# Kernel optimization log

Hardware: AMD Instinct MI355X
Metric: run time of the kernel (lower is better)

The kernel has to match this reference:

```python
import jax, jax.numpy as jnp
import numpy as np

NEG_SLOPE = 0.01


def conv2d_border(x, w, b, stride):
    # replicate ('border') padding of 1, then VALID conv; matches torch padding_mode='border'
    x = jnp.pad(x, ((0, 0), (0, 0), (1, 1), (1, 1)), mode='edge')
    y = jax.lax.conv_general_dilated(x, w, (stride, stride), 'VALID',
                                     dimension_numbers=('NCHW', 'OIHW', 'NCHW'))
    return y + b[None, :, None, None]


def leaky(x):
    return jnp.where(x >= 0, x, NEG_SLOPE * x)


def view_encoder(x, w1, b1, w2, b2, w3, b3):
    x = leaky(conv2d_border(x, w1, b1, 1))
    x = leaky(conv2d_border(x, w2, b2, 2))
    x = leaky(conv2d_border(x, w3, b3, 2))
    return x  # (V, F, H/4, W/4)


def bilinear_gather(nts, uv, vid):
    # nts: (V, F, Hp, Wp); uv: (N, 2) in [0,1]; vid: (N,) int -> (N, F)
    V, Fd, Hp, Wp = nts.shape
    tex = jnp.transpose(nts, (0, 2, 3, 1))  # (V, Hp, Wp, F)
    x = uv[:, 0] * (Wp - 1)
    y = uv[:, 1] * (Hp - 1)
    x0 = jnp.clip(jnp.floor(x).astype(jnp.int32), 0, Wp - 2)
    y0 = jnp.clip(jnp.floor(y).astype(jnp.int32), 0, Hp - 2)
    wx = (x - x0)[:, None]
    wy = (y - y0)[:, None]
    f00 = tex[vid, y0, x0]
    f01 = tex[vid, y0, x0 + 1]
    f10 = tex[vid, y0 + 1, x0]
    f11 = tex[vid, y0 + 1, x0 + 1]
    return (f00 * (1 - wx) * (1 - wy) + f01 * wx * (1 - wy)
            + f10 * (1 - wx) * wy + f11 * wx * wy)


def mha(q, k, v, wq, bq, wk, bk, wv, bv, wo, bo, num_heads):
    # q: (B,1,D), k/v: (B,S,D); torch nn.MultiheadAttention math, batch_first
    B, Lq, D = q.shape
    S = k.shape[1]
    hd = D // num_heads
    qh = (q @ wq.T + bq).reshape(B, Lq, num_heads, hd).transpose(0, 2, 1, 3)
    kh = (k @ wk.T + bk).reshape(B, S, num_heads, hd).transpose(0, 2, 1, 3)
    vh = (v @ wv.T + bv).reshape(B, S, num_heads, hd).transpose(0, 2, 1, 3)
    scores = jnp.einsum('bhqd,bhkd->bhqk', qh, kh) / jnp.sqrt(jnp.float32(hd)).astype(q.dtype)
    attn = jax.nn.softmax(scores, axis=-1)
    out = jnp.einsum('bhqk,bhkd->bhqd', attn, vh)
    out = out.transpose(0, 2, 1, 3).reshape(B, Lq, D)
    return out @ wo.T + bo


def setup_inputs() -> dict:
    key = jax.random.key(0)
    ks = jax.random.split(key, 20)
    V, C, H, W = 8, 3, 512, 512
    B = 262144
    D = 64
    view_tex = jax.random.normal(ks[0], (V, C, H, W), jnp.float32)
    uv = jax.random.uniform(ks[1], (B, 3, 2), jnp.float32)
    vid = jax.random.randint(ks[2], (B, 3, 1), 0, V).astype(jnp.float32)
    uvi = jnp.concatenate([uv, vid], axis=-1)  # (B,3,3)
    raydir = jax.random.normal(ks[3], (B, 3), jnp.float32)

    def winit(k, shape, fan_in):
        return jax.random.normal(k, shape, jnp.float32) / np.sqrt(fan_in)

    params = dict(
        w1=winit(ks[4], (32, C, 3, 3), C * 9), b1=jnp.zeros((32,), jnp.float32),
        w2=winit(ks[5], (64, 32, 3, 3), 32 * 9), b2=jnp.zeros((64,), jnp.float32),
        w3=winit(ks[6], (D, 64, 3, 3), 64 * 9), b3=jnp.zeros((D,), jnp.float32),
        rw1=winit(ks[7], (64, 3), 3), rb1=jnp.zeros((64,), jnp.float32),
        rw2=winit(ks[8], (D, 64), 64), rb2=jnp.zeros((D,), jnp.float32),
        wq=winit(ks[9], (D, D), D), bq=jnp.zeros((D,), jnp.float32),
        wk=winit(ks[10], (D, D), D), bk=jnp.zeros((D,), jnp.float32),
        wv=winit(ks[11], (D, D), D), bv=jnp.zeros((D,), jnp.float32),
        wo=winit(ks[12], (D, D), D), bo=jnp.zeros((D,), jnp.float32),
    )
    return dict(view_tex=view_tex, uvi=uvi, raydir=raydir, **params)


def reference(view_tex, uvi, raydir,
              w1, b1, w2, b2, w3, b3,
              rw1, rb1, rw2, rb2,
              wq, bq, wk, bk, wv, bv, wo, bo):
    NUM_HEADS = 4
    nts = view_encoder(view_tex, w1, b1, w2, b2, w3, b3)  # (V,F,Hp,Wp)
    B = uvi.shape[0]
    uv = uvi[:, :, :2].reshape(B * 3, 2)
    vid = uvi[:, :, 2].astype(jnp.int32).reshape(B * 3)
    feats = bilinear_gather(nts, uv, vid).reshape(B, 3, -1)  # (B,3,F)
    ray_feat = jnp.maximum(raydir @ rw1.T + rb1, 0) @ rw2.T + rb2  # (B,F)
    fused = mha(ray_feat[:, None, :], feats, feats,
                wq, bq, wk, bk, wv, bv, wo, bo, NUM_HEADS)
    return fused[:, 0, :], feats
```

## Files before the change

kernel.cpp:

```cpp
#include <hip/hip_runtime.h>

typedef short s8v __attribute__((ext_vector_type(8)));
typedef short s4v __attribute__((ext_vector_type(4)));
typedef float f4v __attribute__((ext_vector_type(4)));

#define DEV __device__ __forceinline__

DEV short f2bs(float f){
  unsigned int u = __float_as_uint(f);
  u += 0x7fffu + ((u >> 16) & 1u);
  return (short)(u >> 16);
}
DEV float b2f(short s){
  return __uint_as_float(((unsigned int)(unsigned short)s) << 16);
}
DEV float lrelu(float x){ return x >= 0.f ? x : 0.01f*x; }
DEV unsigned pk2(float a, float b){
  return (unsigned)(unsigned short)f2bs(a) | ((unsigned)(unsigned short)f2bs(b) << 16);
}

__global__ __launch_bounds__(256) void k0_prep(
    const float* __restrict__ w1, const float* __restrict__ w2,
    const float* __restrict__ w3, const float* __restrict__ rw2,
    const float* __restrict__ wq, const float* __restrict__ wk,
    const float* __restrict__ wv, const float* __restrict__ wo,
    char* __restrict__ wreg)
{
  int idx = blockIdx.x*256 + threadIdx.x;
  short* w1b = (short*)(wreg);
  short* w2b = (short*)(wreg + 3456);
  short* w3b = (short*)(wreg + 40320);
  short* rw2b = (short*)(wreg + 114048);
  short* wqb  = (short*)(wreg + 122240);
  short* wkb  = (short*)(wreg + 130432);
  short* wvb  = (short*)(wreg + 138624);
  short* wob  = (short*)(wreg + 146816);
  if (idx < 1024){
    int e = idx & 7, l = (idx >> 3) & 63, m = idx >> 9;
    int k = (l >> 4)*8 + e;
    int cout = m*16 + (l & 15);
    w1b[idx] = (k < 27) ? f2bs(w1[cout*27 + k]) : (short)0;
  } else if (idx < 19456){
    int j = idx - 1024;
    int kk = j / 2048, c = (j >> 5) & 63, ci = j & 31;
    w2b[j] = f2bs(w2[c*288 + ci*9 + kk]);
  } else if (idx < 56320){
    int j = idx - 19456;
    int kk = j / 4096, c = (j >> 6) & 63, ci = j & 63;
    w3b[j] = f2bs(w3[c*576 + ci*9 + kk]);
  } else if (idx < 60416){
    int j = idx - 56320; rw2b[j] = f2bs(rw2[j]);
  } else if (idx < 64512){
    int j = idx - 60416; wqb[j] = f2bs(wq[j]);
  } else if (idx < 68608){
    int j = idx - 64512; wkb[j] = f2bs(wk[j]);
  } else if (idx < 72704){
    int j = idx - 68608; wvb[j] = f2bs(wv[j]);
  } else if (idx < 76800){
    int j = idx - 72704; wob[j] = f2bs(wo[j]);
  }
}

__global__ __launch_bounds__(256) void kc12(
    const float* __restrict__ vt, short* __restrict__ c2,
    const short* __restrict__ w1b, const float* __restrict__ b1,
    const short* __restrict__ w2b, const float* __restrict__ b2, int v0)
{
  __shared__ short srcT[3108];
  __shared__ short rb[4][2880];
  const int tid = threadIdx.x;
  const int l = tid & 63, wid = tid >> 6;
  const int p = l & 15, g = l >> 4;
  const int OXB = blockIdx.x*64, OYB = blockIdx.y*2;
  const float* src = vt + (size_t)(v0 + blockIdx.z)*3*512*512;

  #pragma unroll
  for (int it=0; it<13; it++){
    int idx = it*256 + tid;
    if (idx < 3108){
      int ci = idx/1036, rem = idx - ci*1036;
      int row = rem/148, col = rem - row*148;
      int gr = min(max(2*OYB - 2 + row, 0), 511);
      int gc = min(max(2*OXB - 2 + col, 0), 511);
      srcT[idx] = f2bs(src[((size_t)ci*512 + gr)*512 + gc]);
    }
  }

  int boffB[8];
  #pragma unroll
  for (int e=0;e<8;e++){
    int k = g*8 + e;
    int ci = (k*57) >> 9;
    int r9 = k - ci*9;
    int dy = (r9*11) >> 5;
    int dx = r9 - dy*3;
    boffB[e] = (k < 27) ? (ci*1036 + dy*148 + dx) : 0;
  }
  s8v af0 = *(const s8v*)(w1b + l*8);
  s8v af1 = *(const s8v*)(w1b + 512 + l*8);
  f4v cb0 = *(const f4v*)(b1 + g*4);
  f4v cb1 = *(const f4v*)(b1 + 16 + g*4);

  const int dlt = wid >> 1, h = wid & 1;
  const int oy = OYB + dlt;
  const int ox0 = OXB + h*32;
  const int Cw0 = 2*ox0 - 1;
  short* myrb = rb[wid];
  const f4v FZ = {0.f,0.f,0.f,0.f};
  f4v acc[2][4];
  #pragma unroll
  for (int s2=0;s2<2;s2++)
    #pragma unroll
    for (int m=0;m<4;m++) acc[s2][m] = FZ;

  __syncthreads();

  #pragma unroll
  for (int ky=0; ky<3; ky++){
    const int R = min(max(2*oy + ky - 1, 0), 511);
    const int trb = R - 2*OYB + 1;
    const int sbase = trb*148 + 64*h + p;

    #pragma unroll
    for (int s=0; s<5; s++){
      s8v bf;
      #pragma unroll
      for (int e=0;e<8;e++) bf[e] = srcT[boffB[e] + sbase + s*16];
      f4v d0 = __builtin_amdgcn_mfma_f32_16x16x32_bf16(af0, bf, FZ, 0,0,0);
      f4v d1 = __builtin_amdgcn_mfma_f32_16x16x32_bf16(af1, bf, FZ, 0,0,0);
      int wcol = s*16 + p;
      uint2 wa = { pk2(lrelu(d0[0]+cb0[0]), lrelu(d0[1]+cb0[1])),
                   pk2(lrelu(d0[2]+cb0[2]), lrelu(d0[3]+cb0[3])) };
      *(uint2*)(myrb + wcol*36 + g*4) = wa;
      uint2 wb2 = { pk2(lrelu(d1[0]+cb1[0]), lrelu(d1[1]+cb1[1])),
                    pk2(lrelu(d1[2]+cb1[2]), lrelu(d1[3]+cb1[3])) };
      *(uint2*)(myrb + wcol*36 + 16 + g*4) = wb2;
    }

    #pragma unroll
    for (int s2=0; s2<2; s2++){
      const int locox = s2*16 + p;
      #pragma unroll
      for (int kx=0; kx<3; kx++){
        int raw = Cw0 + 2*locox + kx;
        int ri = max(raw, 0) - Cw0;
        uint2 lo2 = *(const uint2*)(myrb + ri*36 + g*8);
        uint2 hi2 = *(const uint2*)(myrb + ri*36 + g*8 + 4);
        uint4 t4 = {lo2.x, lo2.y, hi2.x, hi2.y};
        s8v bf2 = __builtin_bit_cast(s8v, t4);
        #pragma unroll
        for (int m=0;m<4;m++){
          s8v afr = *(const s8v*)(w2b + ((ky*3+kx)*64 + m*16 + p)*32 + g*8);
          acc[s2][m] = __builtin_amdgcn_mfma_f32_16x16x32_bf16(afr, bf2, acc[s2][m], 0,0,0);
        }
      }
    }
  }

  #pragma unroll
  for (int s2=0; s2<2; s2++){
    short* o = c2 + (((size_t)blockIdx.z*256 + oy)*256 + ox0 + s2*16 + p)*64;
    #pragma unroll
    for (int m=0;m<4;m++){
      f4v bb = *(const f4v*)(b2 + m*16 + g*4);
      s4v pk;
      #pragma unroll
      for (int r=0;r<4;r++) pk[r] = f2bs(lrelu(acc[s2][m][r] + bb[r]));
      *(s4v*)(o + m*16 + g*4) = pk;
    }
  }
}

template<int CIN, int TILES>
__global__ __launch_bounds__(256) void conv_mfma(
    const short* __restrict__ src0, short* __restrict__ dst,
    const short* __restrict__ wb, const float* __restrict__ bias,
    int IH, int IW, int OW, int dstV0)
{
  const int l = threadIdx.x & 63, w = threadIdx.x >> 6;
  const int p = l & 15, g = l >> 4;
  const int ox0 = blockIdx.x*(64*TILES) + w*(16*TILES) + p;
  const int oy = blockIdx.y;
  const short* src = src0 + (size_t)blockIdx.z*IH*IW*CIN;
  const f4v FZ = {0.f,0.f,0.f,0.f};
  f4v acc[TILES][4];
  #pragma unroll
  for (int tl=0;tl<TILES;tl++)
    #pragma unroll
    for (int m=0;m<4;m++) acc[tl][m] = FZ;
  #pragma unroll
  for (int ky=0;ky<3;ky++){
    int iy = min(max(2*oy+ky-1, 0), IH-1);
    #pragma unroll
    for (int kx=0;kx<3;kx++){
      #pragma unroll
      for (int ch=0; ch<CIN/32; ch++){
        s8v bfrag[TILES];
        #pragma unroll
        for (int tl=0;tl<TILES;tl++){
          int ix = min(max(2*(ox0 + 16*tl)+kx-1, 0), IW-1);
          bfrag[tl] = *(const s8v*)(src + ((size_t)iy*IW + ix)*CIN + ch*32 + g*8);
        }
        #pragma unroll
        for (int m=0;m<4;m++){
          s8v afrag = *(const s8v*)(wb + ((ky*3+kx)*64 + m*16 + p)*CIN + ch*32 + g*8);
          #pragma unroll
          for (int tl=0;tl<TILES;tl++)
            acc[tl][m] = __builtin_amdgcn_mfma_f32_16x16x32_bf16(afrag, bfrag[tl], acc[tl][m], 0,0,0);
        }
      }
    }
  }
  const int OH = gridDim.y;
  #pragma unroll
  for (int tl=0;tl<TILES;tl++){
    short* o = dst + (((size_t)(dstV0 + blockIdx.z)*OH + oy)*OW + ox0 + 16*tl)*64;
    #pragma unroll
    for (int m=0;m<4;m++){
      f4v bb = *(const f4v*)(bias + m*16 + g*4);
      s4v pk;
      #pragma unroll
      for (int r=0;r<4;r++) pk[r] = f2bs(lrelu(acc[tl][m][r] + bb[r]));
      *(s4v*)(o + m*16 + g*4) = pk;
    }
  }
}

__global__ __launch_bounds__(256) void k4_gather(
    const short* __restrict__ nts, const float* __restrict__ uvi,
    float* __restrict__ outFeats)
{
  int gid = blockIdx.x*256 + threadIdx.x;
  int tk = gid >> 3, c = (gid & 7)*8;
  const float* up = uvi + (size_t)tk*3;
  float u = up[0], v = up[1];
  int vid = (int)up[2];
  float xf = u*127.f, yf = v*127.f;
  int x0 = min(max((int)floorf(xf), 0), 126);
  int y0 = min(max((int)floorf(yf), 0), 126);
  float wx = xf - (float)x0, wy = yf - (float)y0;
  const short* cb = nts + ((size_t)((vid*128 + y0)*128 + x0))*64 + c;
  s8v c00 = *(const s8v*)(cb);
  s8v c01 = *(const s8v*)(cb + 64);
  s8v c10 = *(const s8v*)(cb + 8192);
  s8v c11 = *(const s8v*)(cb + 8192 + 64);
  f4v o0, o1;
  #pragma unroll
  for (int e=0;e<8;e++){
    float a = b2f(c00[e]); a += wx*(b2f(c01[e]) - a);
    float b = b2f(c10[e]); b += wx*(b2f(c11[e]) - b);
    float val = a + wy*(b - a);
    if (e < 4) o0[e] = val; else o1[e-4] = val;
  }
  float* op = outFeats + (size_t)tk*64 + c;
  *(f4v*)op = o0;
  *(f4v*)(op+4) = o1;
}

#define AFRG(W) (*(const s8v*)((W) + (m*16 + p)*64 + kc*32 + g*8))

__global__ __launch_bounds__(256) void k5_attn(
    const float* __restrict__ feats, const float* __restrict__ raydir,
    const float* __restrict__ rw1, const float* __restrict__ rb1,
    const short* __restrict__ rw2b, const float* __restrict__ rb2,
    const short* __restrict__ wqb, const float* __restrict__ bq,
    const short* __restrict__ wkb, const float* __restrict__ bk,
    const short* __restrict__ wvb, const float* __restrict__ bv,
    const short* __restrict__ wob, const float* __restrict__ bo,
    float* __restrict__ outFused)
{
  __shared__ uint4 ldsq[576];
  unsigned int* ldsu = (unsigned int*)ldsq;
  const int l = threadIdx.x & 63, wid = threadIdx.x >> 6;
  const int p = l & 15, g = l >> 4;
  const int pt = blockIdx.x*64 + wid*16 + p;
  const f4v FZ = {0.f,0.f,0.f,0.f};

#define RELAYOUT(H, OB) { \
    _Pragma("unroll") \
    for (int m_=0;m_<4;m_++){ \
      unsigned int lo_ = (unsigned int)(unsigned short)f2bs(H[m_][0]) \
                       | ((unsigned int)(unsigned short)f2bs(H[m_][1])<<16); \
      unsigned int hi_ = (unsigned int)(unsigned short)f2bs(H[m_][2]) \
                       | ((unsigned int)(unsigned short)f2bs(H[m_][3])<<16); \
      int di_ = wid*576 + p*36 + m_*8 + g*2; \
      ldsu[di_] = lo_; ldsu[di_+1] = hi_; \
    } \
    OB[0] = __builtin_bit_cast(s8v, ldsq[wid*144 + p*9 + g]); \
    OB[1] = __builtin_bit_cast(s8v, ldsq[wid*144 + p*9 + 4 + g]); \
  }

  s8v fb[3][2];
  #pragma unroll
  for (int t=0;t<3;t++){
    const float* fp = feats + (size_t)(pt*3+t)*64;
    #pragma unroll
    for (int kc=0;kc<2;kc++){
      f4v a0 = *(const f4v*)(fp + kc*32 + g*8);
      f4v a1 = *(const f4v*)(fp + kc*32 + g*8 + 4);
      s8v tmp;
      #pragma unroll
      for (int e=0;e<4;e++){ tmp[e] = f2bs(a0[e]); tmp[e+4] = f2bs(a1[e]); }
      fb[t][kc] = tmp;
    }
  }

  float rd0 = raydir[(size_t)pt*3+0];
  float rd1 = raydir[(size_t)pt*3+1];
  float rd2 = raydir[(size_t)pt*3+2];
  s8v xb[2];
  #pragma unroll
  for (int kc=0;kc<2;kc++){
    s8v tmp;
    #pragma unroll
    for (int e=0;e<8;e++){
      int j = kc*32 + g*8 + e;
      float hv = fmaxf(rb1[j] + rw1[j*3]*rd0 + rw1[j*3+1]*rd1 + rw1[j*3+2]*rd2, 0.f);
      tmp[e] = f2bs(hv);
    }
    xb[kc] = tmp;
  }

  f4v acc[4];
  #pragma unroll
  for (int m=0;m<4;m++) acc[m] = FZ;
  #pragma unroll
  for (int kc=0;kc<2;kc++){
    #pragma unroll
    for (int m=0;m<4;m++)
      acc[m] = __builtin_amdgcn_mfma_f32_16x16x32_bf16(AFRG(rw2b), xb[kc], acc[m], 0,0,0);
  }
  float rf[4][4];
  #pragma unroll
  for (int m=0;m<4;m++){
    f4v bb = *(const f4v*)(rb2 + m*16 + g*4);
    #pragma unroll
    for (int r=0;r<4;r++) rf[m][r] = acc[m][r] + bb[r];
  }
  RELAYOUT(rf, xb);

  #pragma unroll
  for (int m=0;m<4;m++) acc[m] = FZ;
  #pragma unroll
  for (int kc=0;kc<2;kc++){
    #pragma unroll
    for (int m=0;m<4;m++)
      acc[m] = __builtin_amdgcn_mfma_f32_16x16x32_bf16(AFRG(wqb), xb[kc], acc[m], 0,0,0);
  }
  float qh[4][4];
  #pragma unroll
  for (int m=0;m<4;m++){
    f4v bb = *(const f4v*)(bq + m*16 + g*4);
    #pragma unroll
    for (int r=0;r<4;r++) qh[m][r] = acc[m][r] + bb[r];
  }

  s8v wkf[2][4];
  #pragma unroll
  for (int kc=0;kc<2;kc++)
    #pragma unroll
    for (int m=0;m<4;m++)
      wkf[kc][m] = AFRG(wkb);

  float sc[3][4];
  #pragma unroll
  for (int t=0;t<3;t++){
    f4v ka[4];
    #pragma unroll
    for (int m=0;m<4;m++) ka[m] = FZ;
    #pragma unroll
    for (int kc=0;kc<2;kc++){
      #pragma unroll
      for (int m=0;m<4;m++)
        ka[m] = __builtin_amdgcn_mfma_f32_16x16x32_bf16(wkf[kc][m], fb[t][kc], ka[m], 0,0,0);
    }
    #pragma unroll
    for (int m=0;m<4;m++){
      f4v bb = *(const f4v*)(bk + m*16 + g*4);
      float part = 0.f;
      #pragma unroll
      for (int r=0;r<4;r++) part += qh[m][r]*(ka[m][r] + bb[r]);
      part += __shfl_xor(part, 16, 64);
      part += __shfl_xor(part, 32, 64);
      sc[t][m] = part*0.25f;
    }
  }

  #pragma unroll
  for (int m=0;m<4;m++){
    float mx = fmaxf(fmaxf(sc[0][m], sc[1][m]), sc[2][m]);
    float e0 = __expf(sc[0][m]-mx);
    float e1 = __expf(sc[1][m]-mx);
    float e2 = __expf(sc[2][m]-mx);
    float inv = 1.f/(e0+e1+e2);
    sc[0][m] = e0*inv; sc[1][m] = e1*inv; sc[2][m] = e2*inv;
  }

  s8v wvf[2][4];
  #pragma unroll
  for (int kc=0;kc<2;kc++)
    #pragma unroll
    for (int m=0;m<4;m++)
      wvf[kc][m] = AFRG(wvb);

  float o[4][4];
  #pragma unroll
  for (int m=0;m<4;m++)
    #pragma unroll
    for (int r=0;r<4;r++) o[m][r] = 0.f;
  #pragma unroll
  for (int t=0;t<3;t++){
    f4v va[4];
    #pragma unroll
    for (int m=0;m<4;m++) va[m] = FZ;
    #pragma unroll
    for (int kc=0;kc<2;kc++){
      #pragma unroll
      for (int m=0;m<4;m++)
        va[m] = __builtin_amdgcn_mfma_f32_16x16x32_bf16(wvf[kc][m], fb[t][kc], va[m], 0,0,0);
    }
    #pragma unroll
    for (int m=0;m<4;m++)
      #pragma unroll
      for (int r=0;r<4;r++) o[m][r] += sc[t][m]*va[m][r];
  }
  #pragma unroll
  for (int m=0;m<4;m++){
    f4v bb = *(const f4v*)(bv + m*16 + g*4);
    #pragma unroll
    for (int r=0;r<4;r++) o[m][r] += bb[r];
  }
  RELAYOUT(o, xb);

  #pragma unroll
  for (int m=0;m<4;m++) acc[m] = FZ;
  #pragma unroll
  for (int kc=0;kc<2;kc++){
    #pragma unroll
    for (int m=0;m<4;m++)
      acc[m] = __builtin_amdgcn_mfma_f32_16x16x32_bf16(AFRG(wob), xb[kc], acc[m], 0,0,0);
  }
  #pragma unroll
  for (int m=0;m<4;m++){
    f4v bb = *(const f4v*)(bo + m*16 + g*4);
    f4v res;
    #pragma unroll
    for (int r=0;r<4;r++) res[r] = acc[m][r] + bb[r];
    *(f4v*)(outFused + (size_t)pt*64 + m*16 + g*4) = res;
  }
#undef RELAYOUT
}

extern "C" void kernel_launch(void* const* d_in, const int* in_sizes, int n_in,
                              void* d_out, int out_size, void* d_ws, size_t ws_size,
                              hipStream_t stream)
{
  const float* view_tex = (const float*)d_in[0];
  const float* uvi    = (const float*)d_in[1];
  const float* raydir = (const float*)d_in[2];
  const float* w1 = (const float*)d_in[3];
  const float* b1 = (const float*)d_in[4];
  const float* w2 = (const float*)d_in[5];
  const float* b2 = (const float*)d_in[6];
  const float* w3 = (const float*)d_in[7];
  const float* b3 = (const float*)d_in[8];
  const float* rw1 = (const float*)d_in[9];
  const float* rb1 = (const float*)d_in[10];
  const float* rw2 = (const float*)d_in[11];
  const float* rb2 = (const float*)d_in[12];
  const float* wq = (const float*)d_in[13];
  const float* bq = (const float*)d_in[14];
  const float* wk = (const float*)d_in[15];
  const float* bk = (const float*)d_in[16];
  const float* wv = (const float*)d_in[17];
  const float* bv = (const float*)d_in[18];
  const float* wo = (const float*)d_in[19];
  const float* bo = (const float*)d_in[20];
  float* out = (float*)d_out;

  const int V = in_sizes[0] / (3*512*512);
  const int B = in_sizes[1] / 9;
  const size_t FEATS_OFF = (size_t)B*64;

  const size_t C2F  = (size_t)V*256*256*64*2;
  const size_t C2V  = (size_t)256*256*64*2;
  const size_t NTSB = (size_t)V*128*128*64*2;
  const size_t WREG = 262144;

  char* base = (char*)d_ws;
  bool full = (ws_size >= C2F + NTSB + WREG);

  char *c2, *ntsp, *wreg;
  if (full){
    c2 = base; ntsp = c2 + C2F; wreg = ntsp + NTSB;
  } else {
    c2 = base; ntsp = c2 + C2V; wreg = ntsp + NTSB;
  }
  short* w1b = (short*)(wreg);
  short* w2b = (short*)(wreg + 3456);
  short* w3b = (short*)(wreg + 40320);
  short* rw2b = (short*)(wreg + 114048);
  short* wqb  = (short*)(wreg + 122240);
  short* wkb  = (short*)(wreg + 130432);
  short* wvb  = (short*)(wreg + 138624);
  short* wob  = (short*)(wreg + 146816);

  k0_prep<<<dim3(300),256,0,stream>>>(w1,w2,w3,rw2,wq,wk,wv,wo,wreg);

  if (full){
    kc12<<<dim3(4,128,V),256,0,stream>>>(view_tex,(short*)c2,w1b,b1,w2b,b2,0);
    conv_mfma<64,2><<<dim3(1,128,V),256,0,stream>>>((const short*)c2,(short*)ntsp,w3b,b3,256,256,128,0);
  } else {
    for (int v=0; v<V; v++){
      kc12<<<dim3(4,128,1),256,0,stream>>>(view_tex,(short*)c2,w1b,b1,w2b,b2,v);
      conv_mfma<64,2><<<dim3(1,128,1),256,0,stream>>>((const short*)c2,(short*)ntsp,w3b,b3,256,256,128,v);
    }
  }

  k4_gather<<<dim3((B*3*8)/256),256,0,stream>>>((const short*)ntsp, uvi, out + FEATS_OFF);

  k5_attn<<<dim3(B/64),256,0,stream>>>(out + FEATS_OFF, raydir,
      rw1, rb1, rw2b, rb2, wqb, bq, wkb, bk, wvb, bv, wob, bo, out);
}
```

Baseline: 339.9 us.

## Fuse bilinear gather into attention kernel and fold Wq into ray MLP

Merges the gather kernel into the attention kernel: each block gathers its 64 points' three feature vectors, writes the fp32 feats output, and stages bf16 copies in LDS, so the attention stage no longer re-reads feats from global memory. Separately, a tiny fold kernel precomputes Wq·rw2 and the combined bias, which removes one 64x64 MFMA stage and one LDS relayout per point. The fold changes bf16 rounding order slightly, and the larger LDS buffer may lower occupancy.

```diff
diff --git a/kernel.cpp b/kernel.cpp
--- a/kernel.cpp
+++ b/kernel.cpp
@@ -31,7 +31,6 @@
   short* w2b = (short*)(wreg + 3456);
   short* w3b = (short*)(wreg + 40320);
   short* rw2b = (short*)(wreg + 114048);
-  short* wqb  = (short*)(wreg + 122240);
   short* wkb  = (short*)(wreg + 130432);
   short* wvb  = (short*)(wreg + 138624);
   short* wob  = (short*)(wreg + 146816);
@@ -51,13 +50,37 @@
   } else if (idx < 60416){
     int j = idx - 56320; rw2b[j] = f2bs(rw2[j]);
   } else if (idx < 64512){
-    int j = idx - 60416; wqb[j] = f2bs(wq[j]);
   } else if (idx < 68608){
     int j = idx - 64512; wkb[j] = f2bs(wk[j]);
   } else if (idx < 72704){
     int j = idx - 68608; wvb[j] = f2bs(wv[j]);
   } else if (idx < 76800){
     int j = idx - 72704; wob[j] = f2bs(wo[j]);
+  }
+}
+
+__global__ __launch_bounds__(256) void k0b_fold(
+    const float* __restrict__ wq, const float* __restrict__ rw2,
+    const float* __restrict__ rb2, const float* __restrict__ bq,
+    char* __restrict__ wreg)
+{
+  short* wqrb = (short*)(wreg + 122240);
+  float* bqr  = (float*)(wreg + 155008);
+  int tid = threadIdx.x;
+  int i = tid >> 2, k0 = (tid & 3)*16;
+  #pragma unroll
+  for (int kk=0; kk<16; kk++){
+    int k = k0 + kk;
+    float s = 0.f;
+    #pragma unroll
+    for (int j=0; j<64; j++) s += wq[i*64+j]*rw2[j*64+k];
+    wqrb[i*64+k] = f2bs(s);
+  }
+  if (tid < 64){
+    float s = bq[tid];
+    #pragma unroll
+    for (int j=0; j<64; j++) s += wq[tid*64+j]*rb2[j];
+    bqr[tid] = s;
   }
 }
 
@@ -226,84 +249,70 @@
   }
 }
 
-__global__ __launch_bounds__(256) void k4_gather(
+#define AFRG(W) (*(const s8v*)((W) + (m*16 + p)*64 + kc*32 + g*8))
+
+__global__ __launch_bounds__(256) void k45_fused(
     const short* __restrict__ nts, const float* __restrict__ uvi,
-    float* __restrict__ outFeats)
-{
-  int gid = blockIdx.x*256 + threadIdx.x;
-  int tk = gid >> 3, c = (gid & 7)*8;
-  const float* up = uvi + (size_t)tk*3;
-  float u = up[0], v = up[1];
-  int vid = (int)up[2];
-  float xf = u*127.f, yf = v*127.f;
-  int x0 = min(max((int)floorf(xf), 0), 126);
-  int y0 = min(max((int)floorf(yf), 0), 126);
-  float wx = xf - (float)x0, wy = yf - (float)y0;
-  const short* cb = nts + ((size_t)((vid*128 + y0)*128 + x0))*64 + c;
-  s8v c00 = *(const s8v*)(cb);
-  s8v c01 = *(const s8v*)(cb + 64);
-  s8v c10 = *(const s8v*)(cb + 8192);
-  s8v c11 = *(const s8v*)(cb + 8192 + 64);
-  f4v o0, o1;
-  #pragma unroll
-  for (int e=0;e<8;e++){
-    float a = b2f(c00[e]); a += wx*(b2f(c01[e]) - a);
-    float b = b2f(c10[e]); b += wx*(b2f(c11[e]) - b);
-    float val = a + wy*(b - a);
-    if (e < 4) o0[e] = val; else o1[e-4] = val;
-  }
-  float* op = outFeats + (size_t)tk*64 + c;
-  *(f4v*)op = o0;
-  *(f4v*)(op+4) = o1;
-}
-
-#define AFRG(W) (*(const s8v*)((W) + (m*16 + p)*64 + kc*32 + g*8))
-
-__global__ __launch_bounds__(256) void k5_attn(
-    const float* __restrict__ feats, const float* __restrict__ raydir,
+    const float* __restrict__ raydir,
     const float* __restrict__ rw1, const float* __restrict__ rb1,
-    const short* __restrict__ rw2b, const float* __restrict__ rb2,
-    const short* __restrict__ wqb, const float* __restrict__ bq,
+    const short* __restrict__ wqrb, const float* __restrict__ bqr,
     const short* __restrict__ wkb, const float* __restrict__ bk,
     const short* __restrict__ wvb, const float* __restrict__ bv,
     const short* __restrict__ wob, const float* __restrict__ bo,
-    float* __restrict__ outFused)
+    float* __restrict__ outFused, float* __restrict__ outFeats)
 {
-  __shared__ uint4 ldsq[576];
-  unsigned int* ldsu = (unsigned int*)ldsq;
-  const int l = threadIdx.x & 63, wid = threadIdx.x >> 6;
+  __shared__ short lds_fb[64*3*72];
+  const int tid = threadIdx.x;
+  const int l = tid & 63, wid = tid >> 6;
   const int p = l & 15, g = l >> 4;
-  const int pt = blockIdx.x*64 + wid*16 + p;
+  const int pt0 = blockIdx.x*64;
   const f4v FZ = {0.f,0.f,0.f,0.f};
 
-#define RELAYOUT(H, OB) { \
-    _Pragma("unroll") \
-    for (int m_=0;m_<4;m_++){ \
-      unsigned int lo_ = (unsigned int)(unsigned short)f2bs(H[m_][0]) \
-                       | ((unsigned int)(unsigned short)f2bs(H[m_][1])<<16); \
-      unsigned int hi_ = (unsigned int)(unsigned short)f2bs(H[m_][2]) \
-                       | ((unsigned int)(unsigned short)f2bs(H[m_][3])<<16); \
-      int di_ = wid*576 + p*36 + m_*8 + g*2; \
-      ldsu[di_] = lo_; ldsu[di_+1] = hi_; \
-    } \
-    OB[0] = __builtin_bit_cast(s8v, ldsq[wid*144 + p*9 + g]); \
-    OB[1] = __builtin_bit_cast(s8v, ldsq[wid*144 + p*9 + 4 + g]); \
-  }
+  #pragma unroll
+  for (int i=0; i<6; i++){
+    int ck = i*256 + tid;
+    int ptl = ck/24, rem = ck - ptl*24;
+    int t = rem >> 3, c8 = rem & 7;
+    int pt = pt0 + ptl;
+    const float* up = uvi + (size_t)pt*9 + t*3;
+    float u = up[0], v = up[1];
+    int vid = (int)up[2];
+    float xf = u*127.f, yf = v*127.f;
+    int x0 = min(max((int)floorf(xf), 0), 126);
+    int y0 = min(max((int)floorf(yf), 0), 126);
+    float wx = xf - (float)x0, wy = yf - (float)y0;
+    const short* cb = nts + ((size_t)((vid*128 + y0)*128 + x0))*64 + c8*8;
+    s8v c00 = *(const s8v*)(cb);
+    s8v c01 = *(const s8v*)(cb + 64);
+    s8v c10 = *(const s8v*)(cb + 8192);
+    s8v c11 = *(const s8v*)(cb + 8192 + 64);
+    f4v o0, o1;
+    s8v pk;
+    #pragma unroll
+    for (int e=0;e<8;e++){
+      float a = b2f(c00[e]); a += wx*(b2f(c01[e]) - a);
+      float b = b2f(c10[e]); b += wx*(b2f(c11[e]) - b);
+      float val = a + wy*(b - a);
+      if (e < 4) o0[e] = val; else o1[e-4] = val;
+      pk[e] = f2bs(val);
+    }
+    float* op = outFeats + ((size_t)pt*3 + t)*64 + c8*8;
+    *(f4v*)op = o0;
+    *(f4v*)(op+4) = o1;
+    *(s8v*)(&lds_fb[(ptl*3 + t)*72 + c8*8]) = pk;
+  }
+
+  __syncthreads();
+
+  const int ptl16 = wid*16 + p;
+  const int pt = pt0 + ptl16;
 
   s8v fb[3][2];
   #pragma unroll
-  for (int t=0;t<3;t++){
-    const float* fp = feats + (size_t)(pt*3+t)*64;
-    #pragma unroll
-    for (int kc=0;kc<2;kc++){
-      f4v a0 = *(const f4v*)(fp + kc*32 + g*8);
-      f4v a1 = *(const f4v*)(fp + kc*32 + g*8 + 4);
-      s8v tmp;
-      #pragma unroll
-      for (int e=0;e<4;e++){ tmp[e] = f2bs(a0[e]); tmp[e+4] = f2bs(a1[e]); }
-      fb[t][kc] = tmp;
-    }
-  }
+  for (int t=0;t<3;t++)
+    #pragma unroll
+    for (int kc=0;kc<2;kc++)
+      fb[t][kc] = *(const s8v*)(&lds_fb[(ptl16*3 + t)*72 + kc*32 + g*8]);
 
   float rd0 = raydir[(size_t)pt*3+0];
   float rd1 = raydir[(size_t)pt*3+1];
@@ -328,29 +337,12 @@
   for (int kc=0;kc<2;kc++){
     #pragma unroll
     for (int m=0;m<4;m++)
-      acc[m] = __builtin_amdgcn_mfma_f32_16x16x32_bf16(AFRG(rw2b), xb[kc], acc[m], 0,0,0);
-  }
-  float rf[4][4];
+      acc[m] = __builtin_amdgcn_mfma_f32_16x16x32_bf16(AFRG(wqrb), xb[kc], acc[m], 0,0,0);
+  }
+  float qh[4][4];
   #pragma unroll
   for (int m=0;m<4;m++){
-    f4v bb = *(const f4v*)(rb2 + m*16 + g*4);
-    #pragma unroll
-    for (int r=0;r<4;r++) rf[m][r] = acc[m][r] + bb[r];
-  }
-  RELAYOUT(rf, xb);
-
-  #pragma unroll
-  for (int m=0;m<4;m++) acc[m] = FZ;
-  #pragma unroll
-  for (int kc=0;kc<2;kc++){
-    #pragma unroll
-    for (int m=0;m<4;m++)
-      acc[m] = __builtin_amdgcn_mfma_f32_16x16x32_bf16(AFRG(wqb), xb[kc], acc[m], 0,0,0);
-  }
-  float qh[4][4];
-  #pragma unroll
-  for (int m=0;m<4;m++){
-    f4v bb = *(const f4v*)(bq + m*16 + g*4);
+    f4v bb = *(const f4v*)(bqr + m*16 + g*4);
     #pragma unroll
     for (int r=0;r<4;r++) qh[m][r] = acc[m][r] + bb[r];
   }
@@ -430,7 +422,19 @@
     #pragma unroll
     for (int r=0;r<4;r++) o[m][r] += bb[r];
   }
-  RELAYOUT(o, xb);
+
+  {
+    unsigned* rl = (unsigned*)lds_fb + wid*1728;
+    #pragma unroll
+    for (int m=0;m<4;m++){
+      unsigned lo = pk2(o[m][0], o[m][1]);
+      unsigned hi = pk2(o[m][2], o[m][3]);
+      rl[p*36 + m*8 + g*2] = lo;
+      rl[p*36 + m*8 + g*2 + 1] = hi;
+    }
+    xb[0] = __builtin_bit_cast(s8v, *(uint4*)(rl + p*36 + g*4));
+    xb[1] = __builtin_bit_cast(s8v, *(uint4*)(rl + p*36 + 16 + g*4));
+  }
 
   #pragma unroll
   for (int m=0;m<4;m++) acc[m] = FZ;
@@ -448,7 +452,6 @@
     for (int r=0;r<4;r++) res[r] = acc[m][r] + bb[r];
     *(f4v*)(outFused + (size_t)pt*64 + m*16 + g*4) = res;
   }
-#undef RELAYOUT
 }
 
 extern "C" void kernel_launch(void* const* d_in, const int* in_sizes, int n_in,
@@ -499,13 +502,14 @@
   short* w1b = (short*)(wreg);
   short* w2b = (short*)(wreg + 3456);
   short* w3b = (short*)(wreg + 40320);
-  short* rw2b = (short*)(wreg + 114048);
-  short* wqb  = (short*)(wreg + 122240);
+  short* wqrb = (short*)(wreg + 122240);
   short* wkb  = (short*)(wreg + 130432);
   short* wvb  = (short*)(wreg + 138624);
   short* wob  = (short*)(wreg + 146816);
+  float* bqr  = (float*)(wreg + 155008);
 
   k0_prep<<<dim3(300),256,0,stream>>>(w1,w2,w3,rw2,wq,wk,wv,wo,wreg);
+  k0b_fold<<<dim3(1),256,0,stream>>>(wq, rw2, rb2, bq, wreg);
 
   if (full){
     kc12<<<dim3(4,128,V),256,0,stream>>>(view_tex,(short*)c2,w1b,b1,w2b,b2,0);
@@ -517,8 +521,7 @@
     }
   }
 
-  k4_gather<<<dim3((B*3*8)/256),256,0,stream>>>((const short*)ntsp, uvi, out + FEATS_OFF);
-
-  k5_attn<<<dim3(B/64),256,0,stream>>>(out + FEATS_OFF, raydir,
-      rw1, rb1, rw2b, rb2, wqb, bq, wkb, bk, wvb, bv, wob, bo, out);
-}
+  k45_fused<<<dim3(B/64),256,0,stream>>>((const short*)ntsp, uvi, raydir,
+      rw1, rb1, wqrb, bqr, wkb, bk, wvb, bv, wob, bo,
+      out, out + FEATS_OFF);
+}
```

New measurement: 308.5 us. 1.1x faster.
